# Kernel optimization log

Measured on AMD Instinct MI355X. Metric: run time of the kernel, lower is better.

## Reference

```python
import jax, jax.numpy as jnp
import numpy as np

HIDDEN = 768
INNER = 512
EPS = 1e-5


def setup_inputs() -> dict:
    key = jax.random.key(0)
    ks = jax.random.split(key, 6)
    B, S = 8, 4096
    x = jax.random.normal(ks[0], (B, S, HIDDEN), dtype=jnp.float32)
    W1 = jax.random.normal(ks[1], (INNER, HIDDEN), dtype=jnp.float32) * 0.02
    b1 = jnp.zeros((INNER,), dtype=jnp.float32)
    W2 = jax.random.normal(ks[2], (HIDDEN, INNER), dtype=jnp.float32) * 0.02
    b2 = jnp.zeros((HIDDEN,), dtype=jnp.float32)
    # output_proj: nn.Linear(hidden, hidden)
    bound = 1.0 / np.sqrt(HIDDEN)
    Wo = jax.random.uniform(ks[3], (HIDDEN, HIDDEN), minval=-bound, maxval=bound, dtype=jnp.float32)
    bo = jax.random.uniform(ks[4], (HIDDEN,), minval=-bound, maxval=bound, dtype=jnp.float32)
    # LayerNorm affine params
    gamma = jnp.ones((HIDDEN,), dtype=jnp.float32)
    beta = jnp.zeros((HIDDEN,), dtype=jnp.float32)
    return {"x": x, "W1": W1, "b1": b1, "W2": W2, "b2": b2,
            "Wo": Wo, "bo": bo, "gamma": gamma, "beta": beta}


def reference(x, W1, b1, W2, b2, Wo, bo, gamma, beta):
    # NOTE: the torch module's inner 'TTT update' loop never actually modifies
    # W1/b1/W2/b2 (loss computed, no step applied), so the math per token is
    # independent and fully vectorizable across (batch, seq).
    h = jax.nn.relu(jnp.einsum('bsd,id->bsi', x, W1) + b1)       # [B,S,INNER]
    pred = jnp.einsum('bsi,di->bsd', h, W2) + b2                 # [B,S,HIDDEN]
    out = jnp.einsum('bsd,ed->bse', pred, Wo) + bo               # output_proj
    # LayerNorm over last dim
    mu = jnp.mean(out, axis=-1, keepdims=True)
    var = jnp.mean(jnp.square(out - mu), axis=-1, keepdims=True)
    out = (out - mu) * jax.lax.rsqrt(var + EPS) * gamma + beta
    return out
```

## Files before the change

kernel.cpp:

```cpp
#include <hip/hip_runtime.h>
#include <hip/hip_bf16.h>


#define HIDDEN 768
#define INNER  512

typedef __bf16 bf16_t;
typedef bf16_t bf16x8 __attribute__((ext_vector_type(8)));
typedef bf16_t bf16x4 __attribute__((ext_vector_type(4)));
typedef float  f32x4  __attribute__((ext_vector_type(4)));

__device__ __forceinline__ void async16(const void* g, void* lds) {
  __builtin_amdgcn_global_load_lds(
      (const __attribute__((address_space(1))) unsigned int*)g,
      (__attribute__((address_space(3))) unsigned int*)lds, 16, 0, 0);
}

__global__ __launch_bounds__(256)
void prep(const float* __restrict__ W1, const float* __restrict__ W2,
          const float* __restrict__ Wo, bf16_t* __restrict__ W1b,
          bf16_t* __restrict__ W2t, bf16_t* __restrict__ Wob) {
  __shared__ float T[64][65];
  const int b = blockIdx.x, t = threadIdx.x;

  const float4* src; bf16x4* dst; int base;
  if (b < 24)       { src = (const float4*)W1; dst = (bf16x4*)W1b; base = b * 4096; }
  else if (b < 60)  { src = (const float4*)Wo; dst = (bf16x4*)Wob; base = (b - 24) * 4096; }
  else {
    const int tile = b - 60;
    const int d0 = (tile >> 3) << 6;
    const int i0 = (tile & 7) << 6;
#pragma unroll
    for (int j = 0; j < 4; ++j) {
      const int idx = j * 256 + t;
      const int r = idx >> 4, c4 = idx & 15;
      float4 v = *(const float4*)(W2 + (size_t)(d0 + r) * INNER + i0 + c4 * 4);
      T[r][c4 * 4 + 0] = v.x; T[r][c4 * 4 + 1] = v.y;
      T[r][c4 * 4 + 2] = v.z; T[r][c4 * 4 + 3] = v.w;
    }
    __syncthreads();
    const int i = t & 63, h4 = t >> 6;
    bf16x8 o0, o1;
#pragma unroll
    for (int c = 0; c < 8; ++c) { o0[c] = (bf16_t)T[h4 * 16 + c][i]; o1[c] = (bf16_t)T[h4 * 16 + 8 + c][i]; }
    bf16_t* orow = W2t + (size_t)(i0 + i) * HIDDEN + d0 + h4 * 16;
    *(bf16x8*)orow = o0;
    *(bf16x8*)(orow + 8) = o1;
    return;
  }
#pragma unroll
  for (int i = 0; i < 16; ++i) {
    float4 v = src[base + i * 256 + t];
    bf16x4 o;
    o[0] = (bf16_t)v.x; o[1] = (bf16_t)v.y; o[2] = (bf16_t)v.z; o[3] = (bf16_t)v.w;
    dst[base + i * 256 + t] = o;
  }
}

__global__ __launch_bounds__(256)
void beq_k(const float* __restrict__ Wo, const float* __restrict__ b2,
           const float* __restrict__ bo, float* __restrict__ beq) {
  const int e = blockIdx.x * 4 + (threadIdx.x >> 6);
  const int l = threadIdx.x & 63;
  float s = 0.f;
#pragma unroll
  for (int j = 0; j < 12; ++j) s += Wo[(size_t)e * HIDDEN + j * 64 + l] * b2[j * 64 + l];
#pragma unroll
  for (int off = 1; off < 64; off <<= 1) s += __shfl_xor(s, off, 64);
  if (l == 0) beq[e] = s + bo[e];
}

__global__ __launch_bounds__(256, 1)
void gemm1_fused(const float* __restrict__ x, const bf16_t* __restrict__ W1b,
                 const float* __restrict__ b1, bf16_t* __restrict__ h) {
  constexpr int T = HIDDEN / 64;
  __shared__ __align__(16) float  Af[3][128 * 64];
  __shared__ __align__(16) bf16_t Bs[3][128 * 64];

  const int per = gridDim.x >> 3;
  const int nb  = (blockIdx.x & 7) * per + (blockIdx.x >> 3);
  const int m0  = (nb >> 2) * 128;
  const int n0  = (nb & 3) * 128;

  const int tid = threadIdx.x;
  const int w = tid >> 6, l = tid & 63;
  const int wr = w >> 1, wc = w & 1;
  const int fr = l & 15, fq = l >> 4;

#define STAGE_A(buf, k0)                                                      \
  _Pragma("unroll") for (int i = 0; i < 8; ++i) {                             \
    const int G = i * 256 + tid, row = G >> 4, g = G & 15;                    \
    async16(x + (size_t)(m0 + row) * HIDDEN + (k0) + ((g ^ (row & 15)) << 2), \
            (char*)Af[buf] + (size_t)(i * 256 + w * 64) * 16);                \
  }
#define STAGE_B(buf, k0)                                                      \
  _Pragma("unroll") for (int i = 0; i < 4; ++i) {                             \
    const int G = i * 256 + tid, row = G >> 3, g = G & 7;                     \
    async16(W1b + (size_t)(n0 + row) * HIDDEN + (k0) + ((g ^ (row & 7)) << 3),\
            (char*)Bs[buf] + (size_t)(i * 256 + w * 64) * 16);                \
  }

  STAGE_A(0, 0);  STAGE_B(0, 0);
  STAGE_A(1, 64); STAGE_B(1, 64);
  asm volatile("s_waitcnt vmcnt(12)" ::: "memory");
  __builtin_amdgcn_s_barrier();

  f32x4 acc[4][4] = {};
#pragma unroll
  for (int t = 0; t < T; ++t) {
    const int cur = t % 3;
    if (t + 2 < T) {
      const int nx = (t + 2) % 3;
      STAGE_A(nx, (t + 2) * 64);
      STAGE_B(nx, (t + 2) * 64);
    }
    __builtin_amdgcn_s_setprio(1);
#pragma unroll
    for (int kk = 0; kk < 2; ++kk) {
      bf16x8 ax[4], bx[4];
#pragma unroll
      for (int m = 0; m < 4; ++m) {
        const int row = wr * 64 + m * 16 + fr;
        const int c0 = kk * 8 + fq * 2;
        const int s0 = c0 ^ (row & 15), s1 = (c0 + 1) ^ (row & 15);
        f32x4 p0 = *(const f32x4*)(Af[cur] + row * 64 + s0 * 4);
        f32x4 p1 = *(const f32x4*)(Af[cur] + row * 64 + s1 * 4);
        bf16x8 a;
#pragma unroll
        for (int c = 0; c < 4; ++c) { a[c] = (bf16_t)p0[c]; a[4 + c] = (bf16_t)p1[c]; }
        ax[m] = a;
      }
#pragma unroll
      for (int n = 0; n < 4; ++n) {
        const int row = wc * 64 + n * 16 + fr;
        const int slot = (kk * 4 + fq) ^ (row & 7);
        bx[n] = *(const bf16x8*)((const char*)Bs[cur] + row * 128 + slot * 16);
      }
#pragma unroll
      for (int m = 0; m < 4; ++m)
#pragma unroll
        for (int n = 0; n < 4; ++n)
          acc[m][n] = __builtin_amdgcn_mfma_f32_16x16x32_bf16(ax[m], bx[n], acc[m][n], 0, 0, 0);
    }
    __builtin_amdgcn_s_setprio(0);
    if (t < T - 1) {
      if (t + 2 < T) asm volatile("s_waitcnt vmcnt(12)" ::: "memory");
      else           asm volatile("s_waitcnt vmcnt(0)"  ::: "memory");
      __builtin_amdgcn_s_barrier();
    }
  }
#undef STAGE_A
#undef STAGE_B

  const int orow0 = m0 + wr * 64 + fq * 4;
  const int ocol0 = n0 + wc * 64 + fr;
#pragma unroll
  for (int n = 0; n < 4; ++n) {
    const int col = ocol0 + n * 16;
    const float bv = b1[col];
#pragma unroll
    for (int m = 0; m < 4; ++m)
#pragma unroll
      for (int j = 0; j < 4; ++j)
        h[(size_t)(orow0 + m * 16 + j) * INNER + col] = (bf16_t)fmaxf(acc[m][n][j] + bv, 0.f);
  }
}

template <int N_, int K_, int MODE>
__global__ __launch_bounds__(256, 2)
void gemm_bt(const bf16_t* __restrict__ A, const bf16_t* __restrict__ Bt,
             const float* __restrict__ bias, bf16_t* __restrict__ Cout) {
  constexpr int NT = N_ / 128;
  constexpr int T  = K_ / 64;
  __shared__ __align__(16) bf16_t As[2][128 * 64];
  __shared__ __align__(16) bf16_t Bs[2][128 * 64];

  const int per = gridDim.x >> 3;
  const int nb  = (blockIdx.x & 7) * per + (blockIdx.x >> 3);
  const int m0 = (nb / NT) * 128;
  const int n0 = (nb % NT) * 128;

  const int tid = threadIdx.x;
  const int w = tid >> 6, l = tid & 63;
  const int wr = w >> 1, wc = w & 1;
  const int fr = l & 15, fq = l >> 4;

#define STAGE(dst, src, r0, k0)                                               \
  _Pragma("unroll") for (int i = 0; i < 4; ++i) {                             \
    const int G = i * 256 + tid, row = G >> 3, g = G & 7;                     \
    async16((src) + (size_t)((r0) + row) * K_ + (k0) + ((g ^ (row & 7)) << 3),\
            (char*)(dst) + (size_t)(i * 256 + w * 64) * 16);                  \
  }

  STAGE(As[0], A, m0, 0); STAGE(Bs[0], Bt, n0, 0);
  __syncthreads();

  f32x4 acc[4][4] = {};
#pragma unroll
  for (int t = 0; t < T; ++t) {
    const int cur = t & 1;
    if (t < T - 1) {
      STAGE(As[cur ^ 1], A, m0, (t + 1) * 64);
      STAGE(Bs[cur ^ 1], Bt, n0, (t + 1) * 64);
    }
#pragma unroll
    for (int kk = 0; kk < 2; ++kk) {
      bf16x8 ax[4], bx[4];
#pragma unroll
      for (int m = 0; m < 4; ++m) {
        const int row = wr * 64 + m * 16 + fr;
        const int slot = (kk * 4 + fq) ^ (row & 7);
        ax[m] = *(const bf16x8*)((const char*)As[cur] + row * 128 + slot * 16);
      }
#pragma unroll
      for (int n = 0; n < 4; ++n) {
        const int row = wc * 64 + n * 16 + fr;
        const int slot = (kk * 4 + fq) ^ (row & 7);
        bx[n] = *(const bf16x8*)((const char*)Bs[cur] + row * 128 + slot * 16);
      }
#pragma unroll
      for (int m = 0; m < 4; ++m)
#pragma unroll
        for (int n = 0; n < 4; ++n)
          acc[m][n] = __builtin_amdgcn_mfma_f32_16x16x32_bf16(ax[m], bx[n], acc[m][n], 0, 0, 0);
    }
    __syncthreads();
  }
#undef STAGE

  const int orow0 = m0 + wr * 64 + fq * 4;
  const int ocol0 = n0 + wc * 64 + fr;
#pragma unroll
  for (int n = 0; n < 4; ++n) {
    const int col = ocol0 + n * 16;
    const float bv = (MODE == 2) ? 0.f : bias[col];
#pragma unroll
    for (int m = 0; m < 4; ++m)
#pragma unroll
      for (int j = 0; j < 4; ++j)
        Cout[(size_t)(orow0 + m * 16 + j) * N_ + col] = (bf16_t)(acc[m][n][j] + bv);
  }
}

__global__ __launch_bounds__(256)
void ln_bf16(const bf16_t* __restrict__ raw, const float* __restrict__ gamma,
             const float* __restrict__ beta, float* __restrict__ out) {
  const int r = blockIdx.x * 4 + (threadIdx.x >> 6);
  const int l = threadIdx.x & 63;
  const bf16_t* rp = raw + (size_t)r * HIDDEN;
  float v[12];
  float s = 0.f, q = 0.f;
#pragma unroll
  for (int c = 0; c < 3; ++c) {
    bf16x4 b4 = *(const bf16x4*)(rp + c * 256 + l * 4);
#pragma unroll
    for (int j = 0; j < 4; ++j) {
      const float f = (float)b4[j];
      v[c * 4 + j] = f; s += f; q += f * f;
    }
  }
#pragma unroll
  for (int off = 1; off < 64; off <<= 1) {
    s += __shfl_xor(s, off, 64);
    q += __shfl_xor(q, off, 64);
  }
  const float mu  = s * (1.0f / HIDDEN);
  const float var = fmaxf(q * (1.0f / HIDDEN) - mu * mu, 0.f);
  const float inv = rsqrtf(var + 1e-5f);
  float* op = out + (size_t)r * HIDDEN;
#pragma unroll
  for (int c = 0; c < 3; ++c) {
    float4 g = ((const float4*)gamma)[c * 64 + l];
    float4 b = ((const float4*)beta)[c * 64 + l];
    float4 o;
    o.x = (v[c * 4 + 0] - mu) * inv * g.x + b.x;
    o.y = (v[c * 4 + 1] - mu) * inv * g.y + b.y;
    o.z = (v[c * 4 + 2] - mu) * inv * g.z + b.z;
    o.w = (v[c * 4 + 3] - mu) * inv * g.w + b.w;
    ((float4*)op)[c * 64 + l] = o;
  }
}

extern "C" void kernel_launch(void* const* d_in, const int* in_sizes, int n_in,
                              void* d_out, int out_size, void* d_ws, size_t ws_size,
                              hipStream_t stream) {
  const float* x     = (const float*)d_in[0];
  const float* W1    = (const float*)d_in[1];
  const float* b1    = (const float*)d_in[2];
  const float* W2    = (const float*)d_in[3];
  const float* b2    = (const float*)d_in[4];
  const float* Wo    = (const float*)d_in[5];
  const float* bo    = (const float*)d_in[6];
  const float* gamma = (const float*)d_in[7];
  const float* beta  = (const float*)d_in[8];

  const int M = in_sizes[0] / HIDDEN;

  char* ws = (char*)d_ws;
  bf16_t* raw  = (bf16_t*)ws;
  bf16_t* h    = (bf16_t*)(ws + (size_t)M * HIDDEN * 2);
  bf16_t* W1b  = (bf16_t*)(ws + (size_t)M * HIDDEN * 2 + (size_t)M * INNER * 2);
  bf16_t* W2t  = W1b + INNER * HIDDEN;
  bf16_t* Wob  = W2t + INNER * HIDDEN;
  bf16_t* Weq  = Wob + HIDDEN * HIDDEN;
  float*  beq  = (float*)(Weq + HIDDEN * INNER);

  prep<<<156, 256, 0, stream>>>(W1, W2, Wo, W1b, W2t, Wob);
  beq_k<<<HIDDEN / 4, 256, 0, stream>>>(Wo, b2, bo, beq);

  gemm_bt<INNER, HIDDEN, 2><<<(HIDDEN / 128) * (INNER / 128), 256, 0, stream>>>(Wob, W2t, nullptr, Weq);
  gemm1_fused<<<(M / 128) * (INNER / 128), 256, 0, stream>>>(x, W1b, b1, h);
  gemm_bt<HIDDEN, INNER, 1><<<(M / 128) * (HIDDEN / 128), 256, 0, stream>>>(h, Weq, beq, raw);
  ln_bf16<<<M / 4, 256, 0, stream>>>(raw, gamma, beta, (float*)d_out);
}
```

Before: 150.5 us.

## Replace triple-buffered gemm1 with single-buffer loop and split templated gemm

The first GEMM, which reads fp32 x and casts it to bf16 in-kernel, drops its three-stage async pipeline with manual vmcnt waits and priority hints. It now uses one LDS buffer with barriers around each k-step, a new swizzle pattern, and default launch bounds. The templated gemm_bt is split into two specialized kernels, gemm_weq for the Weq precompute (which also loses the XCD block remap) and gemm2 for the output projection. The smaller LDS footprint may allow more blocks per CU, but global loads no longer overlap with compute inside a block.

New measurement: 137.7 us. -8.5%, faster.

```diff
diff --git a/kernel.cpp b/kernel.cpp
--- a/kernel.cpp
+++ b/kernel.cpp
@@ -70,12 +70,81 @@
   if (l == 0) beq[e] = s + bo[e];
 }
 
-__global__ __launch_bounds__(256, 1)
-void gemm1_fused(const float* __restrict__ x, const bf16_t* __restrict__ W1b,
+__global__ __launch_bounds__(256, 2)
+void gemm_weq(const bf16_t* __restrict__ A, const bf16_t* __restrict__ Bt,
+              bf16_t* __restrict__ Cout) {
+  constexpr int N_ = INNER, K_ = HIDDEN, NT = N_ / 128, T = K_ / 64;
+  __shared__ __align__(16) bf16_t As[2][128 * 64];
+  __shared__ __align__(16) bf16_t Bs[2][128 * 64];
+
+  const int nb = blockIdx.x;
+  const int m0 = (nb / NT) * 128;
+  const int n0 = (nb % NT) * 128;
+
+  const int tid = threadIdx.x;
+  const int w = tid >> 6, l = tid & 63;
+  const int wr = w >> 1, wc = w & 1;
+  const int fr = l & 15, fq = l >> 4;
+
+#define STAGEW(dst, src, r0, k0)                                              \
+  _Pragma("unroll") for (int i = 0; i < 4; ++i) {                             \
+    const int G = i * 256 + tid, row = G >> 3, g = G & 7;                     \
+    async16((src) + (size_t)((r0) + row) * K_ + (k0) + ((g ^ (row & 7)) << 3),\
+            (char*)(dst) + (size_t)(i * 256 + w * 64) * 16);                  \
+  }
+
+  STAGEW(As[0], A, m0, 0); STAGEW(Bs[0], Bt, n0, 0);
+  __syncthreads();
+
+  f32x4 acc[4][4] = {};
+#pragma unroll
+  for (int t = 0; t < T; ++t) {
+    const int cur = t & 1;
+    if (t < T - 1) {
+      STAGEW(As[cur ^ 1], A, m0, (t + 1) * 64);
+      STAGEW(Bs[cur ^ 1], Bt, n0, (t + 1) * 64);
+    }
+#pragma unroll
+    for (int kk = 0; kk < 2; ++kk) {
+      bf16x8 ax[4], bx[4];
+#pragma unroll
+      for (int m = 0; m < 4; ++m) {
+        const int row = wr * 64 + m * 16 + fr;
+        const int slot = (kk * 4 + fq) ^ (row & 7);
+        ax[m] = *(const bf16x8*)((const char*)As[cur] + row * 128 + slot * 16);
+      }
+#pragma unroll
+      for (int n = 0; n < 4; ++n) {
+        const int row = wc * 64 + n * 16 + fr;
+        const int slot = (kk * 4 + fq) ^ (row & 7);
+        bx[n] = *(const bf16x8*)((const char*)Bs[cur] + row * 128 + slot * 16);
+      }
+#pragma unroll
+      for (int m = 0; m < 4; ++m)
+#pragma unroll
+        for (int n = 0; n < 4; ++n)
+          acc[m][n] = __builtin_amdgcn_mfma_f32_16x16x32_bf16(ax[m], bx[n], acc[m][n], 0, 0, 0);
+    }
+    __syncthreads();
+  }
+#undef STAGEW
+
+  const int orow0 = m0 + wr * 64 + fq * 4;
+  const int ocol0 = n0 + wc * 64 + fr;
+#pragma unroll
+  for (int n = 0; n < 4; ++n)
+#pragma unroll
+    for (int m = 0; m < 4; ++m)
+#pragma unroll
+      for (int j = 0; j < 4; ++j)
+        Cout[(size_t)(orow0 + m * 16 + j) * N_ + ocol0 + n * 16] = (bf16_t)acc[m][n][j];
+}
+
+__global__ __launch_bounds__(256)
+void gemm1_xcast(const float* __restrict__ x, const bf16_t* __restrict__ W1b,
                  const float* __restrict__ b1, bf16_t* __restrict__ h) {
-  constexpr int T = HIDDEN / 64;
-  __shared__ __align__(16) float  Af[3][128 * 64];
-  __shared__ __align__(16) bf16_t Bs[3][128 * 64];
+  __shared__ __align__(16) float  Asf[128 * 64];
+  __shared__ __align__(16) bf16_t Bs[128 * 64];
 
   const int per = gridDim.x >> 3;
   const int nb  = (blockIdx.x & 7) * per + (blockIdx.x >> 3);
@@ -87,44 +156,38 @@
   const int wr = w >> 1, wc = w & 1;
   const int fr = l & 15, fq = l >> 4;
 
-#define STAGE_A(buf, k0)                                                      \
-  _Pragma("unroll") for (int i = 0; i < 8; ++i) {                             \
-    const int G = i * 256 + tid, row = G >> 4, g = G & 15;                    \
-    async16(x + (size_t)(m0 + row) * HIDDEN + (k0) + ((g ^ (row & 15)) << 2), \
-            (char*)Af[buf] + (size_t)(i * 256 + w * 64) * 16);                \
-  }
-#define STAGE_B(buf, k0)                                                      \
-  _Pragma("unroll") for (int i = 0; i < 4; ++i) {                             \
-    const int G = i * 256 + tid, row = G >> 3, g = G & 7;                     \
-    async16(W1b + (size_t)(n0 + row) * HIDDEN + (k0) + ((g ^ (row & 7)) << 3),\
-            (char*)Bs[buf] + (size_t)(i * 256 + w * 64) * 16);                \
-  }
-
-  STAGE_A(0, 0);  STAGE_B(0, 0);
-  STAGE_A(1, 64); STAGE_B(1, 64);
-  asm volatile("s_waitcnt vmcnt(12)" ::: "memory");
-  __builtin_amdgcn_s_barrier();
-
   f32x4 acc[4][4] = {};
-#pragma unroll
-  for (int t = 0; t < T; ++t) {
-    const int cur = t % 3;
-    if (t + 2 < T) {
-      const int nx = (t + 2) % 3;
-      STAGE_A(nx, (t + 2) * 64);
-      STAGE_B(nx, (t + 2) * 64);
-    }
-    __builtin_amdgcn_s_setprio(1);
+
+  for (int k0 = 0; k0 < HIDDEN; k0 += 64) {
+    __syncthreads();
+#pragma unroll
+    for (int i = 0; i < 8; ++i) {
+      const int G = i * 256 + tid;
+      const int row = G >> 4, g = G & 15;
+      const int gs = (g & 8) | ((g ^ row) & 7);
+      async16(x + (size_t)(m0 + row) * HIDDEN + k0 + gs * 4,
+              (char*)Asf + (size_t)(i * 256 + w * 64) * 16);
+    }
+#pragma unroll
+    for (int i = 0; i < 4; ++i) {
+      const int G = i * 256 + tid;
+      const int row = G >> 3, g = G & 7;
+      async16(W1b + (size_t)(n0 + row) * HIDDEN + k0 + ((g ^ (row & 7)) << 3),
+              (char*)Bs + (size_t)(i * 256 + w * 64) * 16);
+    }
+    __syncthreads();
+
 #pragma unroll
     for (int kk = 0; kk < 2; ++kk) {
       bf16x8 ax[4], bx[4];
 #pragma unroll
       for (int m = 0; m < 4; ++m) {
         const int row = wr * 64 + m * 16 + fr;
-        const int c0 = kk * 8 + fq * 2;
-        const int s0 = c0 ^ (row & 15), s1 = (c0 + 1) ^ (row & 15);
-        f32x4 p0 = *(const f32x4*)(Af[cur] + row * 64 + s0 * 4);
-        f32x4 p1 = *(const f32x4*)(Af[cur] + row * 64 + s1 * 4);
+        const int g0 = kk * 8 + fq * 2;
+        const int s0 = (g0 & 8) | ((g0 ^ row) & 7);
+        const int s1 = ((g0 + 1) & 8) | (((g0 + 1) ^ row) & 7);
+        f32x4 p0 = *(const f32x4*)(Asf + row * 64 + s0 * 4);
+        f32x4 p1 = *(const f32x4*)(Asf + row * 64 + s1 * 4);
         bf16x8 a;
 #pragma unroll
         for (int c = 0; c < 4; ++c) { a[c] = (bf16_t)p0[c]; a[4 + c] = (bf16_t)p1[c]; }
@@ -134,7 +197,7 @@
       for (int n = 0; n < 4; ++n) {
         const int row = wc * 64 + n * 16 + fr;
         const int slot = (kk * 4 + fq) ^ (row & 7);
-        bx[n] = *(const bf16x8*)((const char*)Bs[cur] + row * 128 + slot * 16);
+        bx[n] = *(const bf16x8*)((const char*)Bs + row * 128 + slot * 16);
       }
 #pragma unroll
       for (int m = 0; m < 4; ++m)
@@ -142,15 +205,7 @@
         for (int n = 0; n < 4; ++n)
           acc[m][n] = __builtin_amdgcn_mfma_f32_16x16x32_bf16(ax[m], bx[n], acc[m][n], 0, 0, 0);
     }
-    __builtin_amdgcn_s_setprio(0);
-    if (t < T - 1) {
-      if (t + 2 < T) asm volatile("s_waitcnt vmcnt(12)" ::: "memory");
-      else           asm volatile("s_waitcnt vmcnt(0)"  ::: "memory");
-      __builtin_amdgcn_s_barrier();
-    }
-  }
-#undef STAGE_A
-#undef STAGE_B
+  }
 
   const int orow0 = m0 + wr * 64 + fq * 4;
   const int ocol0 = n0 + wc * 64 + fr;
@@ -166,12 +221,10 @@
   }
 }
 
-template <int N_, int K_, int MODE>
 __global__ __launch_bounds__(256, 2)
-void gemm_bt(const bf16_t* __restrict__ A, const bf16_t* __restrict__ Bt,
-             const float* __restrict__ bias, bf16_t* __restrict__ Cout) {
-  constexpr int NT = N_ / 128;
-  constexpr int T  = K_ / 64;
+void gemm2(const bf16_t* __restrict__ A, const bf16_t* __restrict__ Bt,
+           const float* __restrict__ bias, bf16_t* __restrict__ Cout) {
+  constexpr int N_ = HIDDEN, K_ = INNER, NT = N_ / 128, T = K_ / 64;
   __shared__ __align__(16) bf16_t As[2][128 * 64];
   __shared__ __align__(16) bf16_t Bs[2][128 * 64];
 
@@ -233,7 +286,7 @@
 #pragma unroll
   for (int n = 0; n < 4; ++n) {
     const int col = ocol0 + n * 16;
-    const float bv = (MODE == 2) ? 0.f : bias[col];
+    const float bv = bias[col];
 #pragma unroll
     for (int m = 0; m < 4; ++m)
 #pragma unroll
@@ -308,8 +361,8 @@
   prep<<<156, 256, 0, stream>>>(W1, W2, Wo, W1b, W2t, Wob);
   beq_k<<<HIDDEN / 4, 256, 0, stream>>>(Wo, b2, bo, beq);
 
-  gemm_bt<INNER, HIDDEN, 2><<<(HIDDEN / 128) * (INNER / 128), 256, 0, stream>>>(Wob, W2t, nullptr, Weq);
-  gemm1_fused<<<(M / 128) * (INNER / 128), 256, 0, stream>>>(x, W1b, b1, h);
-  gemm_bt<HIDDEN, INNER, 1><<<(M / 128) * (HIDDEN / 128), 256, 0, stream>>>(h, Weq, beq, raw);
+  gemm_weq<<<(HIDDEN / 128) * (INNER / 128), 256, 0, stream>>>(Wob, W2t, Weq);
+  gemm1_xcast<<<(M / 128) * (INNER / 128), 256, 0, stream>>>(x, W1b, b1, h);
+  gemm2<<<(M / 128) * (HIDDEN / 128), 256, 0, stream>>>(h, Weq, beq, raw);
   ln_bf16<<<M / 4, 256, 0, stream>>>(raw, gamma, beta, (float*)d_out);
 }
```
